# Kernel optimization log

Measured on AMD Instinct MI355X. Metric: run time of the kernel, lower is better.

## Reference

```python
import jax, jax.numpy as jnp
import numpy as np


def setup_inputs() -> dict:
    key = jax.random.key(0)
    ks = jax.random.split(key, 5)
    B, H, W, C, R = 4, 64, 64, 256, 32
    x = jax.random.normal(ks[0], (B, H, W, C), dtype=jnp.float32)
    # 1x1 conv kernels stored as [C_in, C_out] matrices (equivalent math)
    w_f = jax.random.normal(ks[1], (C, R), dtype=jnp.float32) * (1.0 / np.sqrt(C))
    w_g = jax.random.normal(ks[2], (C, R), dtype=jnp.float32) * (1.0 / np.sqrt(C))
    w_h = jax.random.normal(ks[3], (C, R), dtype=jnp.float32) * (1.0 / np.sqrt(C))
    w_v = jax.random.normal(ks[4], (R, C), dtype=jnp.float32) * (1.0 / np.sqrt(R))
    gamma = jnp.zeros((1,), dtype=jnp.float32)
    return {"x": x, "w_f": w_f, "w_g": w_g, "w_h": w_h, "w_v": w_v, "gamma": gamma}


def reference(x, w_f, w_g, w_h, w_v, gamma):
    B, H, W, C = x.shape
    N = H * W
    xt = x.reshape(B, N, C)                       # flatten spatial tokens
    f = jnp.einsum('bnc,cr->bnr', xt, w_f)        # 1x1 conv == token-wise matmul
    g = jnp.einsum('bnc,cr->bnr', xt, w_g)
    h = jnp.einsum('bnc,cr->bnr', xt, w_h)
    scores = jnp.einsum('bnr,bmr->bnm', f, g)     # [B, N, N]
    # NOTE: original softmaxes over axis=1 (the query/row axis), not axis=-1
    attn = jax.nn.softmax(scores, axis=1)
    y = jnp.einsum('bnm,bmr->bnr', attn, h)       # [B, N, R]
    y = jnp.einsum('bnr,rc->bnc', y, w_v)         # output 1x1 conv
    y = y.reshape(B, H, W, C)
    return gamma * y + x
```

## Files before the change

### kernel.cpp

```cpp
#include <hip/hip_runtime.h>


#define BB 4
#define NN 4096
#define CC 256
#define RR 32
#define LOG2E 1.44269504088896340736f

typedef short short8 __attribute__((ext_vector_type(8)));
typedef short short4v __attribute__((ext_vector_type(4)));
typedef unsigned short ushort8 __attribute__((ext_vector_type(8)));
typedef float floatx4 __attribute__((ext_vector_type(4)));

#define MFMA16 __builtin_amdgcn_mfma_f32_16x16x32_bf16
#define MFMA16K __builtin_amdgcn_mfma_f32_16x16x16bf16_1k

static __device__ __forceinline__ unsigned short f2bf(float f) {
  union { float f; unsigned u; } v; v.f = f;
  const unsigned r = v.u + 0x7fffu + ((v.u >> 16) & 1u);
  return (unsigned short)(r >> 16);
}
static __device__ __forceinline__ unsigned bfpack(float lo, float hi) {
  return __builtin_amdgcn_perm(__float_as_uint(hi), __float_as_uint(lo), 0x07060302u);
}

__global__ __launch_bounds__(256) void k_fgh(
    const float* __restrict__ x, const float* __restrict__ wf,
    const float* __restrict__ wg, const float* __restrict__ wh,
    unsigned short* __restrict__ f16, unsigned short* __restrict__ g16,
    unsigned short* __restrict__ hT16) {
  __shared__ unsigned short wflds[24576];
  const int tid = threadIdx.x, lane = tid & 63, wave = tid >> 6;
  const int col = lane & 15, q = lane >> 4;
  {
    const float* mats[3] = {wf, wg, wh};
#pragma unroll
    for (int mat = 0; mat < 3; ++mat) {
      const float* w = mats[mat];
#pragma unroll 4
      for (int i = 0; i < 32; ++i) {
        const int idx = mat * 8192 + i * 256 + tid;
        const int fid = (idx >> 9) & 15;
        const int kc = fid >> 1, nt = fid & 1;
        const int l2 = (idx >> 3) & 63;
        const int c2 = l2 & 15, q2 = l2 >> 4;
        const int j = idx & 7;
        wflds[idx] = f2bf(w[(kc * 32 + q2 * 8 + j) * RR + nt * 16 + c2]);
      }
    }
  }
  const int t0 = blockIdx.x * 64 + wave * 16;
  short8 af[8];
  const float* xr = x + (long)(t0 + col) * CC + q * 8;
#pragma unroll
  for (int kc = 0; kc < 8; ++kc) {
    float tmp[8];
    *(float4*)(tmp) = *(const float4*)(xr + kc * 32);
    *(float4*)(tmp + 4) = *(const float4*)(xr + kc * 32 + 4);
    short8 o;
#pragma unroll
    for (int j = 0; j < 8; ++j) o[j] = (short)f2bf(tmp[j]);
    af[kc] = o;
  }
  __syncthreads();
  const floatx4 zero = {0.f, 0.f, 0.f, 0.f};
  floatx4 acc[3][2];
#pragma unroll
  for (int m = 0; m < 3; ++m) { acc[m][0] = zero; acc[m][1] = zero; }
#pragma unroll
  for (int kc = 0; kc < 8; ++kc) {
#pragma unroll
    for (int mat = 0; mat < 3; ++mat) {
#pragma unroll
      for (int nt = 0; nt < 2; ++nt) {
        const short8 bf = *(const short8*)(wflds + (mat * 16 + kc * 2 + nt) * 512 + lane * 8);
        acc[mat][nt] = MFMA16(af[kc], bf, acc[mat][nt], 0, 0, 0);
      }
    }
  }
  const int b = t0 >> 12;
#pragma unroll
  for (int nt = 0; nt < 2; ++nt) {
#pragma unroll
    for (int r = 0; r < 4; ++r) {
      const int tok = t0 + q * 4 + r;
      const int n = nt * 16 + col;
      f16[(long)tok * RR + n] = f2bf(acc[0][nt][r] * LOG2E);
      g16[(long)tok * RR + n] = f2bf(acc[1][nt][r]);
      const int tl = tok & (NN - 1);
      const int sp = (tl & ~31) | (q << 3) | ((tl & 16) >> 2) | r;
      hT16[((long)b * RR + n) * NN + sp] = f2bf(acc[2][nt][r]);
    }
  }
}

__global__ __launch_bounds__(256) void k_colsum(
    const unsigned short* __restrict__ f16, const unsigned short* __restrict__ g16,
    float* __restrict__ nlg2cs) {
  __shared__ float red[4][32];
  const int tid = threadIdx.x, lane = tid & 63, wave = tid >> 6;
  const int col = lane & 15, q = lane >> 4;
  const int b = blockIdx.x >> 7;
  const int m0 = (blockIdx.x & 127) * 32;
  const short8 bg1 = *(const short8*)(g16 + ((long)(b * NN + m0 + col)) * RR + q * 8);
  const short8 bg2 = *(const short8*)(g16 + ((long)(b * NN + m0 + 16 + col)) * RR + q * 8);
  const floatx4 zero = {0.f, 0.f, 0.f, 0.f};
  float s1 = 0.f, s2 = 0.f;
  const unsigned short* fb = f16 + ((long)b * NN + wave * (NN / 4)) * RR;
#pragma unroll 4
  for (int n = 0; n < NN / 4; n += 16) {
    const short8 af = *(const short8*)(fb + (long)(n + col) * RR + q * 8);
    const floatx4 d1 = MFMA16(af, bg1, zero, 0, 0, 0);
    const floatx4 d2 = MFMA16(af, bg2, zero, 0, 0, 0);
    s1 += __builtin_amdgcn_exp2f(d1[0]) + __builtin_amdgcn_exp2f(d1[1]) +
          __builtin_amdgcn_exp2f(d1[2]) + __builtin_amdgcn_exp2f(d1[3]);
    s2 += __builtin_amdgcn_exp2f(d2[0]) + __builtin_amdgcn_exp2f(d2[1]) +
          __builtin_amdgcn_exp2f(d2[2]) + __builtin_amdgcn_exp2f(d2[3]);
  }
  s1 += __shfl_xor(s1, 16); s1 += __shfl_xor(s1, 32);
  s2 += __shfl_xor(s2, 16); s2 += __shfl_xor(s2, 32);
  if (lane < 16) {
    red[wave][lane] = s1;
    red[wave][lane + 16] = s2;
  }
  __syncthreads();
  if (tid < 32) {
    const float cs = red[0][tid] + red[1][tid] + red[2][tid] + red[3][tid];
    nlg2cs[(long)b * NN + m0 + tid] = -__builtin_amdgcn_logf(cs);
  }
}

__global__ __launch_bounds__(512, 4) void k_pvout(
    const unsigned short* __restrict__ f16, const unsigned short* __restrict__ g16,
    const unsigned short* __restrict__ hT16, const float* __restrict__ nlg2cs,
    const float* __restrict__ wv, const float* __restrict__ x,
    const float* __restrict__ gamma, float* __restrict__ out) {
  __shared__ float ylds[8][32 * 36];
  __shared__ float sc_all[8][16 * 36];
  __shared__ unsigned short wvlds[8192];
  const int tid = threadIdx.x, lane = tid & 63, wave = tid >> 6;
  const int col = lane & 15, q = lane >> 4;
  const int b = blockIdx.x >> 7;
  const int t0 = (blockIdx.x & 127) * 32;
  const floatx4 zero = {0.f, 0.f, 0.f, 0.f};
  {
#pragma unroll 4
    for (int i = 0; i < 16; ++i) {
      const int idx = i * 512 + tid;
      const int t = idx >> 9;
      const int l2 = (idx >> 3) & 63;
      const int c2 = l2 & 15, q2 = l2 >> 4;
      const int j = idx & 7;
      wvlds[idx] = f2bf(wv[(q2 * 8 + j) * CC + t * 16 + c2]);
    }
  }
  const short8 af1 = *(const short8*)(f16 + ((long)(b * NN + t0 + col)) * RR + q * 8);
  const short8 af2 = *(const short8*)(f16 + ((long)(b * NN + t0 + 16 + col)) * RR + q * 8);
  floatx4 a11 = zero, a12 = zero, a21 = zero, a22 = zero;
  const unsigned short* gb = g16 + (long)b * NN * RR;
  const unsigned short* hb = hT16 + (long)b * RR * NN;
  const float* csb = nlg2cs + (long)b * NN;
  const int mq = wave * 512;
#pragma unroll 2
  for (int mi = 0; mi < 512; mi += 32) {
    const int m0 = mq + mi;
    const short8 bg1 = *(const short8*)(gb + (long)(m0 + col) * RR + q * 8);
    const short8 bg2 = *(const short8*)(gb + (long)(m0 + 16 + col) * RR + q * 8);
    const short8 hv1 = *(const short8*)(hb + (long)col * NN + m0 + q * 8);
    const short8 hv2 = *(const short8*)(hb + (long)(col + 16) * NN + m0 + q * 8);
    const floatx4 cm0 = *(const floatx4*)(csb + m0 + q * 4);
    const floatx4 cm1 = *(const floatx4*)(csb + m0 + 16 + q * 4);
    const floatx4 d00 = MFMA16(bg1, af1, cm0, 0, 0, 0);
    const floatx4 d01 = MFMA16(bg2, af1, cm1, 0, 0, 0);
    const floatx4 d10 = MFMA16(bg1, af2, cm0, 0, 0, 0);
    const floatx4 d11 = MFMA16(bg2, af2, cm1, 0, 0, 0);
    union PU { unsigned u[2]; short4v s; } p00, p01, p10, p11;
    p00.u[0] = bfpack(__builtin_amdgcn_exp2f(d00[0]), __builtin_amdgcn_exp2f(d00[1]));
    p00.u[1] = bfpack(__builtin_amdgcn_exp2f(d00[2]), __builtin_amdgcn_exp2f(d00[3]));
    p01.u[0] = bfpack(__builtin_amdgcn_exp2f(d01[0]), __builtin_amdgcn_exp2f(d01[1]));
    p01.u[1] = bfpack(__builtin_amdgcn_exp2f(d01[2]), __builtin_amdgcn_exp2f(d01[3]));
    p10.u[0] = bfpack(__builtin_amdgcn_exp2f(d10[0]), __builtin_amdgcn_exp2f(d10[1]));
    p10.u[1] = bfpack(__builtin_amdgcn_exp2f(d10[2]), __builtin_amdgcn_exp2f(d10[3]));
    p11.u[0] = bfpack(__builtin_amdgcn_exp2f(d11[0]), __builtin_amdgcn_exp2f(d11[1]));
    p11.u[1] = bfpack(__builtin_amdgcn_exp2f(d11[2]), __builtin_amdgcn_exp2f(d11[3]));
    const short4v bh1lo = __builtin_shufflevector(hv1, hv1, 0, 1, 2, 3);
    const short4v bh1hi = __builtin_shufflevector(hv1, hv1, 4, 5, 6, 7);
    const short4v bh2lo = __builtin_shufflevector(hv2, hv2, 0, 1, 2, 3);
    const short4v bh2hi = __builtin_shufflevector(hv2, hv2, 4, 5, 6, 7);
    a11 = MFMA16K(p00.s, bh1lo, a11, 0, 0, 0);
    a11 = MFMA16K(p01.s, bh1hi, a11, 0, 0, 0);
    a12 = MFMA16K(p00.s, bh2lo, a12, 0, 0, 0);
    a12 = MFMA16K(p01.s, bh2hi, a12, 0, 0, 0);
    a21 = MFMA16K(p10.s, bh1lo, a21, 0, 0, 0);
    a21 = MFMA16K(p11.s, bh1hi, a21, 0, 0, 0);
    a22 = MFMA16K(p10.s, bh2lo, a22, 0, 0, 0);
    a22 = MFMA16K(p11.s, bh2hi, a22, 0, 0, 0);
  }
  {
    float* yp = &ylds[wave][0];
#pragma unroll
    for (int r = 0; r < 4; ++r) {
      yp[(q * 4 + r) * 36 + col] = a11[r];
      yp[(q * 4 + r) * 36 + col + 16] = a12[r];
      yp[(16 + q * 4 + r) * 36 + col] = a21[r];
      yp[(16 + q * 4 + r) * 36 + col + 16] = a22[r];
    }
  }
  __syncthreads();
  {
    const int tile = wave & 1, hh = wave >> 1;
    float s[8] = {0.f, 0.f, 0.f, 0.f, 0.f, 0.f, 0.f, 0.f};
#pragma unroll
    for (int w2 = 0; w2 < 8; ++w2) {
      const float* yp = &ylds[w2][(tile * 16 + col) * 36 + q * 8];
      const float4 u0 = *(const float4*)yp;
      const float4 u1 = *(const float4*)(yp + 4);
      s[0] += u0.x; s[1] += u0.y; s[2] += u0.z; s[3] += u0.w;
      s[4] += u1.x; s[5] += u1.y; s[6] += u1.z; s[7] += u1.w;
    }
    short8 ay;
#pragma unroll
    for (int j = 0; j < 8; ++j) ay[j] = (short)f2bf(s[j]);
    const float gm = gamma[0];
    float* sc = &sc_all[wave][0];
    const int row = lane >> 2, c4 = (lane & 3) * 4;
#pragma unroll
    for (int tp = 0; tp < 4; tp += 2) {
      const short8 bw0 = *(const short8*)(wvlds + (hh * 4 + tp) * 512 + lane * 8);
      const short8 bw1 = *(const short8*)(wvlds + (hh * 4 + tp + 1) * 512 + lane * 8);
      const floatx4 d0 = MFMA16(ay, bw0, zero, 0, 0, 0);
      const floatx4 d1 = MFMA16(ay, bw1, zero, 0, 0, 0);
#pragma unroll
      for (int r = 0; r < 4; ++r) {
        sc[(q * 4 + r) * 36 + col] = d0[r];
        sc[(q * 4 + r) * 36 + col + 16] = d1[r];
      }
#pragma unroll
      for (int j = 0; j < 2; ++j) {
        const float4 v = *(const float4*)(sc + row * 36 + c4 + j * 16);
        const long gidx = (long)(b * NN + t0 + tile * 16 + row) * CC +
                          hh * 64 + tp * 16 + j * 16 + c4;
        const float4 xv = *(const float4*)(x + gidx);
        float4 o;
        o.x = gm * v.x + xv.x; o.y = gm * v.y + xv.y;
        o.z = gm * v.z + xv.z; o.w = gm * v.w + xv.w;
        *(float4*)(out + gidx) = o;
      }
    }
  }
}

extern "C" void kernel_launch(void* const* d_in, const int* in_sizes, int n_in,
                              void* d_out, int out_size, void* d_ws, size_t ws_size,
                              hipStream_t stream) {
  const float* x = (const float*)d_in[0];
  const float* wf = (const float*)d_in[1];
  const float* wg = (const float*)d_in[2];
  const float* wh = (const float*)d_in[3];
  const float* wv = (const float*)d_in[4];
  const float* gamma = (const float*)d_in[5];
  float* out = (float*)d_out;

  unsigned short* f16 = (unsigned short*)d_ws;
  unsigned short* g16 = f16 + (long)BB * NN * RR;
  unsigned short* hT16 = g16 + (long)BB * NN * RR;
  float* nlg2cs = (float*)(hT16 + (long)BB * NN * RR);

  k_fgh<<<BB * NN / 64, 256, 0, stream>>>(x, wf, wg, wh, f16, g16, hT16);
  k_colsum<<<BB * NN / 32, 256, 0, stream>>>(f16, g16, nlg2cs);
  k_pvout<<<BB * 128, 512, 0, stream>>>(f16, g16, hT16, nlg2cs, wv, x, gamma, out);
}
```

Measured before the change: 132.1 us.

## Precompute bf16 weight fragments once and enlarge pvout blocks to 64 tokens

Result: faster. 126.5 us (-4.3%).

```diff
diff --git a/kernel.cpp b/kernel.cpp
--- a/kernel.cpp
+++ b/kernel.cpp
@@ -24,31 +24,41 @@
   return __builtin_amdgcn_perm(__float_as_uint(hi), __float_as_uint(lo), 0x07060302u);
 }
 
+__global__ __launch_bounds__(256) void k_prep(
+    const float* __restrict__ wf, const float* __restrict__ wg,
+    const float* __restrict__ wh, const float* __restrict__ wv,
+    unsigned short* __restrict__ wfrag, unsigned short* __restrict__ wvfrag) {
+  const int idx = blockIdx.x * 256 + threadIdx.x;
+  const int lane = (idx >> 3) & 63;
+  const int j = idx & 7;
+  const int col = lane & 15, q = lane >> 4;
+  if (idx < 24576) {
+    const int mat = idx >> 13;
+    const int fid = (idx >> 9) & 15;
+    const int kc = fid >> 1, nt = fid & 1;
+    const float* w = (mat == 0) ? wf : ((mat == 1) ? wg : wh);
+    wfrag[idx] = f2bf(w[(kc * 32 + q * 8 + j) * RR + nt * 16 + col]);
+  } else {
+    const int r = idx - 24576;
+    const int t = (r >> 9) & 15;
+    wvfrag[r] = f2bf(wv[(q * 8 + j) * CC + t * 16 + col]);
+  }
+}
+
 __global__ __launch_bounds__(256) void k_fgh(
-    const float* __restrict__ x, const float* __restrict__ wf,
-    const float* __restrict__ wg, const float* __restrict__ wh,
+    const float* __restrict__ x, const unsigned short* __restrict__ wfrag,
     unsigned short* __restrict__ f16, unsigned short* __restrict__ g16,
     unsigned short* __restrict__ hT16) {
   __shared__ unsigned short wflds[24576];
   const int tid = threadIdx.x, lane = tid & 63, wave = tid >> 6;
   const int col = lane & 15, q = lane >> 4;
   {
-    const float* mats[3] = {wf, wg, wh};
-#pragma unroll
-    for (int mat = 0; mat < 3; ++mat) {
-      const float* w = mats[mat];
-#pragma unroll 4
-      for (int i = 0; i < 32; ++i) {
-        const int idx = mat * 8192 + i * 256 + tid;
-        const int fid = (idx >> 9) & 15;
-        const int kc = fid >> 1, nt = fid & 1;
-        const int l2 = (idx >> 3) & 63;
-        const int c2 = l2 & 15, q2 = l2 >> 4;
-        const int j = idx & 7;
-        wflds[idx] = f2bf(w[(kc * 32 + q2 * 8 + j) * RR + nt * 16 + c2]);
-      }
-    }
-  }
+    const uint4* src = (const uint4*)wfrag;
+    uint4* dst = (uint4*)wflds;
+#pragma unroll
+    for (int i = 0; i < 12; ++i) dst[tid + i * 256] = src[tid + i * 256];
+  }
+  __syncthreads();
   const int t0 = blockIdx.x * 64 + wave * 16;
   short8 af[8];
   const float* xr = x + (long)(t0 + col) * CC + q * 8;
@@ -62,7 +72,6 @@
     for (int j = 0; j < 8; ++j) o[j] = (short)f2bf(tmp[j]);
     af[kc] = o;
   }
-  __syncthreads();
   const floatx4 zero = {0.f, 0.f, 0.f, 0.f};
   floatx4 acc[3][2];
 #pragma unroll
@@ -130,40 +139,30 @@
   }
 }
 
-__global__ __launch_bounds__(512, 4) void k_pvout(
+__global__ __launch_bounds__(1024, 4) void k_pvout(
     const unsigned short* __restrict__ f16, const unsigned short* __restrict__ g16,
     const unsigned short* __restrict__ hT16, const float* __restrict__ nlg2cs,
-    const float* __restrict__ wv, const float* __restrict__ x,
+    const unsigned short* __restrict__ wvfrag, const float* __restrict__ x,
     const float* __restrict__ gamma, float* __restrict__ out) {
-  __shared__ float ylds[8][32 * 36];
-  __shared__ float sc_all[8][16 * 36];
-  __shared__ unsigned short wvlds[8192];
+  __shared__ float ylds[8][64 * 36];
+  __shared__ float sc_all[16][16 * 36];
   const int tid = threadIdx.x, lane = tid & 63, wave = tid >> 6;
   const int col = lane & 15, q = lane >> 4;
-  const int b = blockIdx.x >> 7;
-  const int t0 = (blockIdx.x & 127) * 32;
+  const int b = blockIdx.x >> 6;
+  const int t0 = (blockIdx.x & 63) * 64;
+  const int tokh = wave & 1, mq = wave >> 1;
+  const int tw = t0 + tokh * 32;
   const floatx4 zero = {0.f, 0.f, 0.f, 0.f};
-  {
-#pragma unroll 4
-    for (int i = 0; i < 16; ++i) {
-      const int idx = i * 512 + tid;
-      const int t = idx >> 9;
-      const int l2 = (idx >> 3) & 63;
-      const int c2 = l2 & 15, q2 = l2 >> 4;
-      const int j = idx & 7;
-      wvlds[idx] = f2bf(wv[(q2 * 8 + j) * CC + t * 16 + c2]);
-    }
-  }
-  const short8 af1 = *(const short8*)(f16 + ((long)(b * NN + t0 + col)) * RR + q * 8);
-  const short8 af2 = *(const short8*)(f16 + ((long)(b * NN + t0 + 16 + col)) * RR + q * 8);
+  const short8 af1 = *(const short8*)(f16 + ((long)(b * NN + tw + col)) * RR + q * 8);
+  const short8 af2 = *(const short8*)(f16 + ((long)(b * NN + tw + 16 + col)) * RR + q * 8);
   floatx4 a11 = zero, a12 = zero, a21 = zero, a22 = zero;
   const unsigned short* gb = g16 + (long)b * NN * RR;
   const unsigned short* hb = hT16 + (long)b * RR * NN;
   const float* csb = nlg2cs + (long)b * NN;
-  const int mq = wave * 512;
+  const int mqb = mq * 512;
 #pragma unroll 2
   for (int mi = 0; mi < 512; mi += 32) {
-    const int m0 = mq + mi;
+    const int m0 = mqb + mi;
     const short8 bg1 = *(const short8*)(gb + (long)(m0 + col) * RR + q * 8);
     const short8 bg2 = *(const short8*)(gb + (long)(m0 + 16 + col) * RR + q * 8);
     const short8 hv1 = *(const short8*)(hb + (long)col * NN + m0 + q * 8);
@@ -197,7 +196,7 @@
     a22 = MFMA16K(p11.s, bh2hi, a22, 0, 0, 0);
   }
   {
-    float* yp = &ylds[wave][0];
+    float* yp = &ylds[mq][(tokh * 32) * 36];
 #pragma unroll
     for (int r = 0; r < 4; ++r) {
       yp[(q * 4 + r) * 36 + col] = a11[r];
@@ -208,7 +207,7 @@
   }
   __syncthreads();
   {
-    const int tile = wave & 1, hh = wave >> 1;
+    const int tile = wave & 3, hh = wave >> 2;
     float s[8] = {0.f, 0.f, 0.f, 0.f, 0.f, 0.f, 0.f, 0.f};
 #pragma unroll
     for (int w2 = 0; w2 < 8; ++w2) {
@@ -226,8 +225,8 @@
     const int row = lane >> 2, c4 = (lane & 3) * 4;
 #pragma unroll
     for (int tp = 0; tp < 4; tp += 2) {
-      const short8 bw0 = *(const short8*)(wvlds + (hh * 4 + tp) * 512 + lane * 8);
-      const short8 bw1 = *(const short8*)(wvlds + (hh * 4 + tp + 1) * 512 + lane * 8);
+      const short8 bw0 = *(const short8*)(wvfrag + (hh * 4 + tp) * 512 + lane * 8);
+      const short8 bw1 = *(const short8*)(wvfrag + (hh * 4 + tp + 1) * 512 + lane * 8);
       const floatx4 d0 = MFMA16(ay, bw0, zero, 0, 0, 0);
       const floatx4 d1 = MFMA16(ay, bw1, zero, 0, 0, 0);
 #pragma unroll
@@ -264,9 +263,12 @@
   unsigned short* f16 = (unsigned short*)d_ws;
   unsigned short* g16 = f16 + (long)BB * NN * RR;
   unsigned short* hT16 = g16 + (long)BB * NN * RR;
-  float* nlg2cs = (float*)(hT16 + (long)BB * NN * RR);
-
-  k_fgh<<<BB * NN / 64, 256, 0, stream>>>(x, wf, wg, wh, f16, g16, hT16);
+  unsigned short* wfrag = hT16 + (long)BB * NN * RR;
+  unsigned short* wvfrag = wfrag + 24576;
+  float* nlg2cs = (float*)(wvfrag + 8192);
+
+  k_prep<<<128, 256, 0, stream>>>(wf, wg, wh, wv, wfrag, wvfrag);
+  k_fgh<<<BB * NN / 64, 256, 0, stream>>>(x, wfrag, f16, g16, hT16);
   k_colsum<<<BB * NN / 32, 256, 0, stream>>>(f16, g16, nlg2cs);
-  k_pvout<<<BB * 128, 512, 0, stream>>>(f16, g16, hT16, nlg2cs, wv, x, gamma, out);
-}
+  k_pvout<<<BB * 64, 1024, 0, stream>>>(f16, g16, hT16, nlg2cs, wvfrag, x, gamma, out);
+}
```
